# Kernel optimization log

Hardware: AMD Instinct MI355X
Metric: run time of the kernel (lower is better)

## Reference

```python
import jax, jax.numpy as jnp
import numpy as np

NUM_HEADS = 4
NUM_GROUPS = 8
EPS = 1e-5


def setup_inputs() -> dict:
    key = jax.random.key(0)
    ks = jax.random.split(key, 4)
    b, c, h, w = 16, 512, 32, 32
    x = jax.random.normal(ks[0], (b, c, h, w), dtype=jnp.float32)
    norm_gamma = jnp.ones((c,), dtype=jnp.float32)
    norm_beta = jnp.zeros((c,), dtype=jnp.float32)
    qkv_w = jax.random.normal(ks[1], (3 * c, c), dtype=jnp.float32) * (c ** -0.5)
    qkv_b = jnp.zeros((3 * c,), dtype=jnp.float32)
    proj_w = jax.random.normal(ks[2], (c, c), dtype=jnp.float32) * (c ** -0.5)
    proj_b = jnp.zeros((c,), dtype=jnp.float32)
    return {"x": x, "norm_gamma": norm_gamma, "norm_beta": norm_beta,
            "qkv_w": qkv_w, "qkv_b": qkv_b, "proj_w": proj_w, "proj_b": proj_b}


def reference(x, norm_gamma, norm_beta, qkv_w, qkv_b, proj_w, proj_b):
    b, c, h, w = x.shape
    nh = NUM_HEADS
    dh = c // nh
    n = h * w
    # GroupNorm(8, c): normalize over (c/G, h, w) within each group, biased var
    xg = x.reshape(b, NUM_GROUPS, -1)
    mu = jnp.mean(xg, axis=-1, keepdims=True)
    var = jnp.var(xg, axis=-1, keepdims=True)
    xn = ((xg - mu) * jax.lax.rsqrt(var + EPS)).reshape(b, c, h, w)
    xn = xn * norm_gamma[:, None, None] + norm_beta[:, None, None]
    # QKV 1x1 conv == channel matmul
    qkv = jnp.einsum('oc,bchw->bohw', qkv_w, xn) + qkv_b[:, None, None]
    q, k, v = jnp.split(qkv, 3, axis=1)  # each [b, c, h, w]

    def to_heads(t):  # [b, c, h, w] -> [b, nh, n, dh]
        return t.reshape(b, nh, dh, n).transpose(0, 1, 3, 2)

    q, k, v = to_heads(q), to_heads(k), to_heads(v)
    scale = dh ** -0.5
    attn = jax.nn.softmax(jnp.einsum('bhnd,bhmd->bhnm', q, k) * scale, axis=-1)
    out = jnp.einsum('bhnm,bhmd->bhnd', attn, v)  # [b, nh, n, dh]
    out = out.transpose(0, 1, 3, 2).reshape(b, c, h, w)
    out = jnp.einsum('oc,bchw->bohw', proj_w, out) + proj_b[:, None, None]
    return x + out
```

## Files before the change

### kernel.cpp

```cpp
#include <hip/hip_runtime.h>

typedef unsigned short u16;
typedef unsigned int   u32;

typedef __attribute__((ext_vector_type(8)))  short bf16x8;
typedef __attribute__((ext_vector_type(16))) float f32x16;
typedef __attribute__((ext_vector_type(2)))  unsigned int u32x2;
#define MFMA32(a, b, c) __builtin_amdgcn_mfma_f32_32x32x16_bf16(a, b, c, 0, 0, 0)

__device__ __forceinline__ float bf2f(u16 h) { return __uint_as_float(((u32)h) << 16); }
__device__ __forceinline__ u16 f2bf(float f) {
  u32 u = __float_as_uint(f);
  u += 0x7fffu + ((u >> 16) & 1u);
  return (u16)(u >> 16);
}
__device__ __forceinline__ void unpack8(uint4 u, float* f) {
  f[0] = __uint_as_float(u.x << 16); f[1] = __uint_as_float(u.x & 0xffff0000u);
  f[2] = __uint_as_float(u.y << 16); f[3] = __uint_as_float(u.y & 0xffff0000u);
  f[4] = __uint_as_float(u.z << 16); f[5] = __uint_as_float(u.z & 0xffff0000u);
  f[6] = __uint_as_float(u.w << 16); f[7] = __uint_as_float(u.w & 0xffff0000u);
}
__device__ __forceinline__ void unpack4(uint2 u, float* f) {
  f[0] = __uint_as_float(u.x << 16); f[1] = __uint_as_float(u.x & 0xffff0000u);
  f[2] = __uint_as_float(u.y << 16); f[3] = __uint_as_float(u.y & 0xffff0000u);
}

template <bool F>
__device__ __forceinline__ void load8(const void* p, size_t idx, float* f) {
  if constexpr (F) {
    const float4* q = (const float4*)((const float*)p + idx);
    float4 a = q[0], b = q[1];
    f[0] = a.x; f[1] = a.y; f[2] = a.z; f[3] = a.w;
    f[4] = b.x; f[5] = b.y; f[6] = b.z; f[7] = b.w;
  } else {
    unpack8(*(const uint4*)((const u16*)p + idx), f);
  }
}
template <bool F>
__device__ __forceinline__ void load4(const void* p, size_t idx, float* f) {
  if constexpr (F) {
    float4 a = *(const float4*)((const float*)p + idx);
    f[0] = a.x; f[1] = a.y; f[2] = a.z; f[3] = a.w;
  } else {
    unpack4(*(const uint2*)((const u16*)p + idx), f);
  }
}
template <bool F>
__device__ __forceinline__ float load1(const void* p, size_t idx) {
  if constexpr (F) return ((const float*)p)[idx];
  else return bf2f(((const u16*)p)[idx]);
}

__device__ __forceinline__ void gl2lds16(const void* g, void* l) {
  __builtin_amdgcn_global_load_lds(
      (const __attribute__((address_space(1))) void*)g,
      (__attribute__((address_space(3))) void*)l, 16, 0, 0);
}

__global__ void detect_dtype(const void* __restrict__ x, int* __restrict__ flag) {
  if (threadIdx.x == 0 && blockIdx.x == 0) {
    const u32* p = (const u32*)x;
    int sane = 0;
    for (int i = 0; i < 256; ++i) {
      u32 e = (p[i] >> 7) & 0xFFu;
      sane += (e >= 100u && e <= 150u) ? 1 : 0;
    }
    *flag = (sane < 192) ? 1 : 0;
  }
}

__global__ void signal_ws(u16* __restrict__ out, int n) {
  int i = blockIdx.x * 256 + threadIdx.x;
  if (i < n) out[i] = 0x42C8;
}

#define SM_SCALE 0.08838834764831843f
#define QSC 0.12751743f


__global__ void __launch_bounds__(256) wconv_rt(const void* __restrict__ qkvw,
                                                const void* __restrict__ qkvb,
                                                u16* __restrict__ dst,
                                                const int* __restrict__ flag) {
  const bool F = (flag[0] != 0);
  int i = (blockIdx.x * 256 + threadIdx.x) * 8;
  if (i >= 787968) return;
  if (!F) {
    uint4 v = (i < 786432) ? *(const uint4*)((const u16*)qkvw + i)
                           : *(const uint4*)((const u16*)qkvb + (i - 786432));
    *(uint4*)(dst + i) = v;
  } else {
    const float* src = (i < 786432) ? ((const float*)qkvw + i)
                                    : ((const float*)qkvb + (i - 786432));
    float f[8];
    float4 a = *(const float4*)src, b = *(const float4*)(src + 4);
    f[0]=a.x; f[1]=a.y; f[2]=a.z; f[3]=a.w; f[4]=b.x; f[5]=b.y; f[6]=b.z; f[7]=b.w;
    u32 w0 = (u32)f2bf(f[0]) | ((u32)f2bf(f[1]) << 16);
    u32 w1 = (u32)f2bf(f[2]) | ((u32)f2bf(f[3]) << 16);
    u32 w2 = (u32)f2bf(f[4]) | ((u32)f2bf(f[5]) << 16);
    u32 w3 = (u32)f2bf(f[6]) | ((u32)f2bf(f[7]) << 16);
    *(uint4*)(dst + i) = make_uint4(w0, w1, w2, w3);
  }
}

template <bool F>
__device__ __forceinline__ void gn_norm_body(
    const void* __restrict__ x, const void* __restrict__ gamma,
    const void* __restrict__ beta, u16* __restrict__ xT,
    int g, int b, int tid,
    float* ssum, float* ssq, float* scb, float* bsb, float (*Tf)[65]) {
  const size_t base = (size_t)(b * 512 + g * 64) * 1024;
  float sum = 0.f, sq = 0.f;
  for (int i = tid; i < 8192; i += 256) {
    float f[8]; load8<F>(x, base + (size_t)i * 8, f);
#pragma unroll
    for (int m = 0; m < 8; ++m) { sum += f[m]; sq += f[m] * f[m]; }
  }
  ssum[tid] = sum; ssq[tid] = sq; __syncthreads();
  for (int off = 128; off > 0; off >>= 1) {
    if (tid < off) { ssum[tid] += ssum[tid + off]; ssq[tid] += ssq[tid + off]; }
    __syncthreads();
  }
  if (tid < 64) {
    float mu  = ssum[0] * (1.f / 65536.f);
    float var = ssq[0] * (1.f / 65536.f) - mu * mu;
    float s = load1<F>(gamma, g * 64 + tid) * rsqrtf(var + 1e-5f);
    scb[tid] = s;
    bsb[tid] = load1<F>(beta, g * 64 + tid) - mu * s;
  }
  __syncthreads();

  for (int s0 = 0; s0 < 1024; s0 += 64) {
#pragma unroll
    for (int half = 0; half < 2; ++half) {
      int idx = tid + half * 256;
      int c_loc = idx >> 3, s8 = (idx & 7) * 8;
      float f[8];
      load8<F>(x, base + (size_t)c_loc * 1024 + s0 + s8, f);
      float sm = scb[c_loc], ba = bsb[c_loc];
#pragma unroll
      for (int m = 0; m < 8; ++m) Tf[s8 + m][c_loc] = f[m] * sm + ba;
    }
    __syncthreads();
#pragma unroll
    for (int half = 0; half < 2; ++half) {
      int idx = tid + half * 256;
      int s_loc = idx >> 3, c8 = (idx & 7) * 8;
      u32 pk[4];
#pragma unroll
      for (int m = 0; m < 4; ++m)
        pk[m] = (u32)f2bf(Tf[s_loc][c8 + 2 * m]) |
                ((u32)f2bf(Tf[s_loc][c8 + 2 * m + 1]) << 16);
      *(uint4*)(xT + (size_t)(b * 1024 + s0 + s_loc) * 512 + g * 64 + c8) =
          make_uint4(pk[0], pk[1], pk[2], pk[3]);
    }
    __syncthreads();
  }
}

__global__ void __launch_bounds__(256) gn_norm_rt(const void* __restrict__ x,
                                                  const void* __restrict__ gamma,
                                                  const void* __restrict__ beta,
                                                  u16* __restrict__ xT,
                                                  const int* __restrict__ flag) {
  __shared__ float ssum[256], ssq[256], scb[64], bsb[64];
  __shared__ float Tf[64][65];
  const int g = blockIdx.x, b = blockIdx.y, tid = threadIdx.x;
  if (flag[0] != 0) gn_norm_body<true >(x, gamma, beta, xT, g, b, tid, ssum, ssq, scb, bsb, Tf);
  else              gn_norm_body<false>(x, gamma, beta, xT, g, b, tid, ssum, ssq, scb, bsb, Tf);
}

__global__ void __launch_bounds__(256, 4)
gemm_qkv(const u16* __restrict__ xT, const u16* __restrict__ wbf,
         u16* __restrict__ qkT, u16* __restrict__ Vbuf) {
  const bool vrole = (blockIdx.y >= 8);
  const int n0 = blockIdx.x * 128;
  const int m0 = (vrole ? (int)blockIdx.y - 8 : (int)blockIdx.y) * 128;
  const int b  = blockIdx.z;
  __shared__ __align__(16) u16 At[8192];
  __shared__ __align__(16) u16 Bt[8192];
  const int tid = threadIdx.x;
  const int w = tid >> 6, lane = tid & 63;
  const int lo = lane & 31, hi = lane >> 5;
  const int wm = w >> 1, wn = w & 1;
  const u16* bias = wbf + 786432;
  const u16* Ab = vrole ? (wbf + 524288) : (xT + (size_t)b * 524288);
  const u16* Bb = vrole ? (xT + (size_t)b * 524288) : wbf;
  u16* outp = vrole ? (Vbuf + (size_t)b * 524288) : (qkT + (size_t)b * 1048576);
  const int srow = lane >> 3, spc = lane & 7;

  f32x16 cA[2][2];
#pragma unroll
  for (int i = 0; i < 2; ++i)
#pragma unroll
    for (int j = 0; j < 2; ++j)
#pragma unroll
      for (int r = 0; r < 16; ++r) cA[i][j][r] = 0.f;

  for (int kt = 0; kt < 8; ++kt) {
    const int kb = kt * 64;
#pragma unroll
    for (int c = 0; c < 4; ++c) {
      int grp = w * 4 + c;
      int row = grp * 8 + srow;
      int lc  = spc ^ (row & 7);
      gl2lds16(Ab + (size_t)(m0 + row) * 512 + kb + lc * 8, &At[grp * 512]);
      gl2lds16(Bb + (size_t)(n0 + row) * 512 + kb + lc * 8, &Bt[grp * 512]);
    }
    __syncthreads();
#pragma unroll
    for (int k16 = 0; k16 < 4; ++k16) {
      const int lc = k16 * 2 + hi;
      const int rA0 = wm * 64 + lo,  rA1 = rA0 + 32;
      const int rB0 = wn * 64 + lo,  rB1 = rB0 + 32;
      bf16x8 a0 = *(const bf16x8*)&At[rA0 * 64 + ((lc ^ (rA0 & 7)) << 3)];
      bf16x8 a1 = *(const bf16x8*)&At[rA1 * 64 + ((lc ^ (rA1 & 7)) << 3)];
      bf16x8 b0 = *(const bf16x8*)&Bt[rB0 * 64 + ((lc ^ (rB0 & 7)) << 3)];
      bf16x8 b1 = *(const bf16x8*)&Bt[rB1 * 64 + ((lc ^ (rB1 & 7)) << 3)];
      cA[0][0] = MFMA32(a0, b0, cA[0][0]);
      cA[0][1] = MFMA32(a0, b1, cA[0][1]);
      cA[1][0] = MFMA32(a1, b0, cA[1][0]);
      cA[1][1] = MFMA32(a1, b1, cA[1][1]);
    }
    __syncthreads();
  }

  float bcol[2] = {0.f, 0.f};
  if (!vrole) {
    bcol[0] = bf2f(bias[n0 + wn * 64 + lo]);
    bcol[1] = bf2f(bias[n0 + wn * 64 + 32 + lo]);
  }
#pragma unroll
  for (int mt = 0; mt < 2; ++mt)
#pragma unroll
    for (int nt = 0; nt < 2; ++nt) {
      const int nbase = n0 + wn * 64 + nt * 32;
#pragma unroll
      for (int r = 0; r < 16; ++r) {
        int m = m0 + wm * 64 + mt * 32 + (r & 3) + 8 * (r >> 2) + 4 * hi;
        int n = nbase + lo;
        float v = cA[mt][nt][r];
        if (!vrole) {
          v += bcol[nt];
          if (nbase < 512) v *= QSC;
        } else {
          v += bf2f(bias[1024 + m]);
        }
        outp[(size_t)m * 1024 + n] = f2bf(v);
      }
    }
}

template <bool F>
__device__ __forceinline__ void proj_body(const void* __restrict__ A,
                                          const u16* __restrict__ B,
                                          const void* __restrict__ bias,
                                          const void* __restrict__ resid,
                                          void* __restrict__ outp,
                                          int n0, int m0, int b, int tid,
                                          u16 (*At)[72], u16 (*Bt)[72]) {
  const int w = tid >> 6, lane = tid & 63;
  const int lo = lane & 31, hi = lane >> 5;
  const int wm = w >> 1, wn = w & 1;
  const size_t bBase = (size_t)b * 524288;

  f32x16 cA[2][2];
#pragma unroll
  for (int i = 0; i < 2; ++i)
#pragma unroll
    for (int j = 0; j < 2; ++j)
#pragma unroll
      for (int r = 0; r < 16; ++r) cA[i][j][r] = 0.f;

  for (int kt = 0; kt < 8; ++kt) {
#pragma unroll
    for (int i = 0; i < 4; ++i) {
      int idx = tid + i * 256;
      int row = idx >> 3, kc = (idx & 7) * 8;
      int k = kt * 64 + kc;
      {
        if constexpr (F) {
          float f[8]; load8<true>(A, (size_t)(m0 + row) * 512 + k, f);
          u32 w0 = (u32)f2bf(f[0]) | ((u32)f2bf(f[1]) << 16);
          u32 w1 = (u32)f2bf(f[2]) | ((u32)f2bf(f[3]) << 16);
          u32 w2 = (u32)f2bf(f[4]) | ((u32)f2bf(f[5]) << 16);
          u32 w3 = (u32)f2bf(f[6]) | ((u32)f2bf(f[7]) << 16);
          *(uint4*)&At[row][kc] = make_uint4(w0, w1, w2, w3);
        } else {
          *(uint4*)&At[row][kc] =
              *(const uint4*)((const u16*)A + (size_t)(m0 + row) * 512 + k);
        }
      }
      *(uint4*)&Bt[row][kc] =
          *(const uint4*)(B + bBase + (size_t)(n0 + row) * 512 + k);
    }
    __syncthreads();
#pragma unroll
    for (int k16 = 0; k16 < 4; ++k16) {
      const int ko = k16 * 16 + hi * 8;
      bf16x8 a0 = *(const bf16x8*)&At[wm * 64 + lo][ko];
      bf16x8 a1 = *(const bf16x8*)&At[wm * 64 + 32 + lo][ko];
      bf16x8 b0 = *(const bf16x8*)&Bt[wn * 64 + lo][ko];
      bf16x8 b1 = *(const bf16x8*)&Bt[wn * 64 + 32 + lo][ko];
      cA[0][0] = MFMA32(a0, b0, cA[0][0]);
      cA[0][1] = MFMA32(a0, b1, cA[0][1]);
      cA[1][0] = MFMA32(a1, b0, cA[1][0]);
      cA[1][1] = MFMA32(a1, b1, cA[1][1]);
    }
    __syncthreads();
  }

#pragma unroll
  for (int mt = 0; mt < 2; ++mt)
#pragma unroll
    for (int nt = 0; nt < 2; ++nt) {
#pragma unroll
      for (int r = 0; r < 16; ++r) {
        int m = m0 + wm * 64 + mt * 32 + (r & 3) + 8 * (r >> 2) + 4 * hi;
        int n = n0 + wn * 64 + nt * 32 + lo;
        float v = cA[mt][nt][r];
        v += load1<F>(bias, m);
        v += load1<F>(resid, bBase + (size_t)m * 1024 + n);
        size_t off = bBase + (size_t)m * 1024 + n;
        if constexpr (F) ((float*)outp)[off] = v;
        else             ((u16*)outp)[off] = f2bf(v);
      }
    }
}

__global__ void __launch_bounds__(256, 4)
proj_rt(const void* __restrict__ projw, const u16* __restrict__ aout,
        const void* __restrict__ projb, const void* __restrict__ x,
        void* __restrict__ outp, const int* __restrict__ flag) {
  __shared__ __align__(16) u16 At[128][72];
  __shared__ __align__(16) u16 Bt[128][72];
  const int n0 = blockIdx.x * 128, m0 = blockIdx.y * 128, b = blockIdx.z;
  if (flag[0] != 0) proj_body<true >(projw, aout, projb, x, outp, n0, m0, b, threadIdx.x, At, Bt);
  else              proj_body<false>(projw, aout, projb, x, outp, n0, m0, b, threadIdx.x, At, Bt);
}

__global__ void __launch_bounds__(256, 2) attn4(const u16* __restrict__ qkT,
                                                const u16* __restrict__ V,
                                                u16* __restrict__ aout) {
  const int bh = blockIdx.x;
  const int q0 = blockIdx.y * 128;
  const int b = bh >> 2, h = bh & 3;
  const u16* qt = qkT + (size_t)b * 1048576;
  const u16* vb = V + (size_t)b * 524288 + (size_t)(h * 128) * 1024;
  __shared__ __align__(16) u16 smem[32768];
  const int tid = threadIdx.x;
  const int w = tid >> 6, lane = tid & 63;
  const int lo = lane & 31, hi = lane >> 5;

#pragma unroll
  for (int c = 0; c < 8; ++c) {
    int grp = w * 8 + c;
    int row = grp * 4 + (lane >> 4);
    int lc  = (lane & 15) ^ (row & 7);
    gl2lds16(qt + (size_t)(q0 + row) * 1024 + h * 128 + lc * 8, &smem[grp * 512]);
  }
#pragma unroll
  for (int c = 0; c < 4; ++c) {
    int grp = w * 4 + c;
    { int row = grp * 4 + (lane >> 4);
      int lc  = (lane & 15) ^ (row & 7);
      gl2lds16(qt + (size_t)row * 1024 + 512 + h * 128 + lc * 8,
               &smem[16384 + grp * 512]); }
    { int row = grp * 8 + (lane >> 3);
      int lc  = (lane & 7) ^ (row & 7);
      gl2lds16(vb + (size_t)row * 1024 + lc * 8,
               &smem[16384 + 8192 + grp * 512]); }
  }
  __syncthreads();
  bf16x8 qf[8];
  {
    const int row = 32 * w + lo;
#pragma unroll
    for (int k16 = 0; k16 < 8; ++k16) {
      int lc = k16 * 2 + hi;
      qf[k16] = *(const bf16x8*)&smem[row * 128 + ((lc ^ (row & 7)) << 3)];
    }
  }
  __syncthreads();

  f32x16 o[4];
  float lp = 0.f;
#pragma unroll
  for (int dt = 0; dt < 4; ++dt)
#pragma unroll
    for (int r = 0; r < 16; ++r) o[dt][r] = 0.f;

  for (int kt = 0; kt < 16; ++kt) {
    const u16* rb = &smem[((kt & 1) ^ 1) << 14];
    u16* wbuf = &smem[(kt & 1) << 14];

    if (kt < 15) {
      const int k0n = (kt + 1) * 64;
#pragma unroll
      for (int c = 0; c < 4; ++c) {
        int grp = w * 4 + c;
        { int row = grp * 4 + (lane >> 4);
          int lc  = (lane & 15) ^ (row & 7);
          gl2lds16(qt + (size_t)(k0n + row) * 1024 + 512 + h * 128 + lc * 8,
                   wbuf + grp * 512); }
        { int row = grp * 8 + (lane >> 3);
          int lc  = (lane & 7) ^ (row & 7);
          gl2lds16(vb + (size_t)row * 1024 + k0n + lc * 8,
                   wbuf + 8192 + grp * 512); }
      }
    }

    f32x16 s0, s1;
#pragma unroll
    for (int r = 0; r < 16; ++r) { s0[r] = 0.f; s1[r] = 0.f; }
    __builtin_amdgcn_s_setprio(1);
#pragma unroll
    for (int k16 = 0; k16 < 8; ++k16) {
      const int lc = k16 * 2 + hi;
      const int r0 = lo, r1 = lo + 32;
      bf16x8 kf0 = *(const bf16x8*)&rb[r0 * 128 + ((lc ^ (r0 & 7)) << 3)];
      bf16x8 kf1 = *(const bf16x8*)&rb[r1 * 128 + ((lc ^ (r1 & 7)) << 3)];
      s0 = MFMA32(kf0, qf[k16], s0);
      s1 = MFMA32(kf1, qf[k16], s1);
    }
    __builtin_amdgcn_s_setprio(0);

#pragma unroll
    for (int r = 0; r < 16; ++r) {
      s0[r] = exp2f(s0[r]);
      s1[r] = exp2f(s1[r]);
      lp += s0[r] + s1[r];
    }

    bf16x8 pa[4];
#define MKPA(ps, rb0, dst) do {                                               \
      u32 qa0, qa1, qb0, qb1;                                                 \
      asm("v_cvt_pk_bf16_f32 %0, %1, %2" : "=v"(qa0)                          \
          : "v"((ps)[(rb0) + 0]), "v"((ps)[(rb0) + 1]));                      \
      asm("v_cvt_pk_bf16_f32 %0, %1, %2" : "=v"(qa1)                          \
          : "v"((ps)[(rb0) + 2]), "v"((ps)[(rb0) + 3]));                      \
      asm("v_cvt_pk_bf16_f32 %0, %1, %2" : "=v"(qb0)                          \
          : "v"((ps)[(rb0) + 4]), "v"((ps)[(rb0) + 5]));                      \
      asm("v_cvt_pk_bf16_f32 %0, %1, %2" : "=v"(qb1)                          \
          : "v"((ps)[(rb0) + 6]), "v"((ps)[(rb0) + 7]));                      \
      u32x2 r0 = __builtin_amdgcn_permlane32_swap(qa0, qb0, false, false);    \
      u32x2 r1 = __builtin_amdgcn_permlane32_swap(qa1, qb1, false, false);    \
      union { u32 u[4]; bf16x8 v8; } pk_;                                     \
      pk_.u[0] = r0[0]; pk_.u[1] = r1[0]; pk_.u[2] = r0[1]; pk_.u[3] = r1[1]; \
      dst = pk_.v8;                                                           \
    } while (0)
    MKPA(s0, 0, pa[0]);
    MKPA(s0, 8, pa[1]);
    MKPA(s1, 0, pa[2]);
    MKPA(s1, 8, pa[3]);
#undef MKPA

    __builtin_amdgcn_s_setprio(1);
#pragma unroll
    for (int t = 0; t < 4; ++t) {
      const int lc = t * 2 + hi;
#pragma unroll
      for (int dt = 0; dt < 4; ++dt) {
        const int row = dt * 32 + lo;
        bf16x8 bv = *(const bf16x8*)&rb[8192 + row * 64 + ((lc ^ (row & 7)) << 3)];
        o[dt] = MFMA32(pa[t], bv, o[dt]);
      }
    }
    __builtin_amdgcn_s_setprio(0);
    __syncthreads();
  }

  float linv = 1.f / (lp + __shfl_xor(lp, 32));
#pragma unroll
  for (int r = 0; r < 16; ++r) {
    int pat = (r & 3) + 8 * (r >> 2) + 4 * hi;
    float lr = __shfl(linv, pat);
    int q = q0 + 32 * w + pat;
    size_t base = (size_t)(b * 1024 + q) * 512 + h * 128;
    aout[base +  0 + lo] = f2bf(o[0][r] * lr);
    aout[base + 32 + lo] = f2bf(o[1][r] * lr);
    aout[base + 64 + lo] = f2bf(o[2][r] * lr);
    aout[base + 96 + lo] = f2bf(o[3][r] * lr);
  }
}


template <bool F>
__global__ void __launch_bounds__(256) gn_stats(const void* __restrict__ x,
                                                const void* __restrict__ gamma,
                                                const void* __restrict__ beta,
                                                float* __restrict__ sc,
                                                float* __restrict__ bs,
                                                const int* __restrict__ flag) {
  if ((flag[0] != 0) != F) return;
  const int g = blockIdx.x, b = blockIdx.y;
  const int tid = threadIdx.x;
  const size_t base = (size_t)(b * 512 + g * 64) * 1024;
  float sum = 0.f, sq = 0.f;
  for (int i = tid; i < 8192; i += 256) {
    float f[8]; load8<F>(x, base + (size_t)i * 8, f);
#pragma unroll
    for (int m = 0; m < 8; ++m) { sum += f[m]; sq += f[m] * f[m]; }
  }
  __shared__ float ssum[256], ssq[256];
  ssum[tid] = sum; ssq[tid] = sq; __syncthreads();
  for (int off = 128; off > 0; off >>= 1) {
    if (tid < off) { ssum[tid] += ssum[tid + off]; ssq[tid] += ssq[tid + off]; }
    __syncthreads();
  }
  if (tid < 64) {
    float mu  = ssum[0] * (1.f / 65536.f);
    float var = ssq[0] * (1.f / 65536.f) - mu * mu;
    int c = g * 64 + tid;
    float s = load1<F>(gamma, c) * rsqrtf(var + 1e-5f);
    sc[b * 512 + c] = s;
    bs[b * 512 + c] = load1<F>(beta, c) - mu * s;
  }
}

template <bool F, bool BEXT, bool FOUT>
__global__ void __launch_bounds__(256) gemm64(const void* __restrict__ A,
                                              const void* __restrict__ B,
                                              const float* __restrict__ sc,
                                              const float* __restrict__ bs,
                                              const void* __restrict__ bias,
                                              const void* __restrict__ resid,
                                              void* __restrict__ outp,
                                              int mrows, int donorm, int bstride,
                                              const int* __restrict__ flag) {
  if ((flag[0] != 0) != F) return;
  const int s0 = blockIdx.x * 64;
  const int o0 = blockIdx.y * 64;
  const int b  = blockIdx.z;
  __shared__ __align__(16) float At[64][36];
  __shared__ __align__(16) float Bt[64][36];
  const int tid = threadIdx.x;
  const int ty = tid >> 4, tx = tid & 15;
  const int i0 = ty * 4, j0 = tx * 4;
  const int arow = tid >> 2, akc = (tid & 3) * 8;
  const int brow = tid >> 3, bnc = (tid & 7) * 8;
  float acc[4][4] = {};

  for (int kt = 0; kt < 512; kt += 32) {
    float af[8];
    load8<F>(A, (size_t)(o0 + arow) * 512 + akc + kt, af);
    *(float4*)&At[arow][akc]     = make_float4(af[0], af[1], af[2], af[3]);
    *(float4*)&At[arow][akc + 4] = make_float4(af[4], af[5], af[6], af[7]);
    const int c = kt + brow;
    float bf[8];
    load8<(BEXT && F)>(B, (size_t)(b * bstride + c) * 1024 + s0 + bnc, bf);
    float smul = 1.f, badd = 0.f;
    if (donorm) { smul = sc[b * 512 + c]; badd = bs[b * 512 + c]; }
#pragma unroll
    for (int m = 0; m < 8; ++m) Bt[bnc + m][brow] = bf[m] * smul + badd;
    __syncthreads();
#pragma unroll
    for (int kq = 0; kq < 8; ++kq) {
      float4 a0 = *(const float4*)&At[i0 + 0][kq * 4];
      float4 a1 = *(const float4*)&At[i0 + 1][kq * 4];
      float4 a2 = *(const float4*)&At[i0 + 2][kq * 4];
      float4 a3 = *(const float4*)&At[i0 + 3][kq * 4];
      float4 c0 = *(const float4*)&Bt[j0 + 0][kq * 4];
      float4 c1 = *(const float4*)&Bt[j0 + 1][kq * 4];
      float4 c2 = *(const float4*)&Bt[j0 + 2][kq * 4];
      float4 c3 = *(const float4*)&Bt[j0 + 3][kq * 4];
#define DOT4(ii, jj, AV, CV) acc[ii][jj] += AV.x * CV.x + AV.y * CV.y + AV.z * CV.z + AV.w * CV.w;
      DOT4(0,0,a0,c0) DOT4(0,1,a0,c1) DOT4(0,2,a0,c2) DOT4(0,3,a0,c3)
      DOT4(1,0,a1,c0) DOT4(1,1,a1,c1) DOT4(1,2,a1,c2) DOT4(1,3,a1,c3)
      DOT4(2,0,a2,c0) DOT4(2,1,a2,c1) DOT4(2,2,a2,c2) DOT4(2,3,a2,c3)
      DOT4(3,0,a3,c0) DOT4(3,1,a3,c1) DOT4(3,2,a3,c2) DOT4(3,3,a3,c3)
#undef DOT4
    }
    __syncthreads();
  }
#pragma unroll
  for (int ii = 0; ii < 4; ++ii) {
    const int o = o0 + i0 + ii;
    const float bb = load1<F>(bias, o);
    float v[4];
#pragma unroll
    for (int jj = 0; jj < 4; ++jj) v[jj] = acc[ii][jj] + bb;
    if (resid) {
      float xf[4];
      load4<F>(resid, (size_t)(b * 512 + o) * 1024 + s0 + j0, xf);
#pragma unroll
      for (int jj = 0; jj < 4; ++jj) v[jj] += xf[jj];
    }
    const size_t ooff = (size_t)(b * mrows + o) * 1024 + s0 + j0;
    if constexpr (FOUT) {
      *(float4*)((float*)outp + ooff) = make_float4(v[0], v[1], v[2], v[3]);
    } else {
      uint2 pk;
      pk.x = (u32)f2bf(v[0]) | ((u32)f2bf(v[1]) << 16);
      pk.y = (u32)f2bf(v[2]) | ((u32)f2bf(v[3]) << 16);
      *(uint2*)((u16*)outp + ooff) = pk;
    }
  }
}

__global__ void __launch_bounds__(256, 2) attn_old(u16* __restrict__ qkv) {
  const int q0 = blockIdx.x * 128;
  const int bh = blockIdx.y;
  const int b = bh >> 2, h = bh & 3;
  u16* qp = qkv + (size_t)(b * 1536 + h * 128) * 1024;
  const u16* kp = qp + (size_t)512 * 1024;
  const u16* vp = qp + (size_t)1024 * 1024;
  __shared__ __align__(16) u16 Qt[128][136];
  __shared__ __align__(16) u16 Kt[32][136];
  __shared__ __align__(16) u16 Vt[128][40];
  __shared__ __align__(16) u16 Pt[128][40];
  const int tid = threadIdx.x;
  const int w = tid >> 6, lane = tid & 63;
  const int lo = lane & 31, hi = lane >> 5;

  for (int idx = tid; idx < 2048; idx += 256) {
    int d = idx >> 4, s8 = (idx & 15) * 8;
    uint4 qv = *(const uint4*)(qp + (size_t)d * 1024 + q0 + s8);
    const u16* qs = (const u16*)&qv;
#pragma unroll
    for (int m = 0; m < 8; ++m) Qt[s8 + m][d] = qs[m];
  }
  __syncthreads();
  bf16x8 qf[8];
#pragma unroll
  for (int kq = 0; kq < 8; ++kq)
    qf[kq] = *(const bf16x8*)&Qt[32 * w + lo][kq * 16 + hi * 8];

  f32x16 o0, o1, o2, o3;
  float lp[16];
#pragma unroll
  for (int r = 0; r < 16; ++r) { o0[r] = 0.f; o1[r] = 0.f; o2[r] = 0.f; o3[r] = 0.f; lp[r] = 0.f; }

  for (int kt = 0; kt < 32; ++kt) {
    const int k0 = kt * 32;
    __syncthreads();
    for (int idx = tid; idx < 512; idx += 256) {
      int d = idx >> 2, s8 = (idx & 3) * 8;
      uint4 kv = *(const uint4*)(kp + (size_t)d * 1024 + k0 + s8);
      const u16* ks = (const u16*)&kv;
#pragma unroll
      for (int m = 0; m < 8; ++m) Kt[s8 + m][d] = ks[m];
      *(uint4*)&Vt[d][s8] = *(const uint4*)(vp + (size_t)d * 1024 + k0 + s8);
    }
    __syncthreads();
    f32x16 acc;
#pragma unroll
    for (int r = 0; r < 16; ++r) acc[r] = 0.f;
#pragma unroll
    for (int kq = 0; kq < 8; ++kq) {
      bf16x8 bq = *(const bf16x8*)&Kt[lo][kq * 16 + hi * 8];
      acc = MFMA32(qf[kq], bq, acc);
    }
#pragma unroll
    for (int r = 0; r < 16; ++r) {
      float pe = __expf(acc[r] * SM_SCALE);
      lp[r] += pe;
      int row = (r & 3) + 8 * (r >> 2) + 4 * hi;
      Pt[32 * w + row][lo] = f2bf(pe);
    }
    __syncthreads();
#pragma unroll
    for (int kq2 = 0; kq2 < 2; ++kq2) {
      bf16x8 a2 = *(const bf16x8*)&Pt[32 * w + lo][kq2 * 16 + hi * 8];
      bf16x8 b0 = *(const bf16x8*)&Vt[ 0 + lo][kq2 * 16 + hi * 8];
      bf16x8 b1 = *(const bf16x8*)&Vt[32 + lo][kq2 * 16 + hi * 8];
      bf16x8 b2 = *(const bf16x8*)&Vt[64 + lo][kq2 * 16 + hi * 8];
      bf16x8 b3 = *(const bf16x8*)&Vt[96 + lo][kq2 * 16 + hi * 8];
      o0 = MFMA32(a2, b0, o0);
      o1 = MFMA32(a2, b1, o1);
      o2 = MFMA32(a2, b2, o2);
      o3 = MFMA32(a2, b3, o3);
    }
  }
#pragma unroll
  for (int r = 0; r < 16; ++r) {
    float su = lp[r];
    su += __shfl_xor(su, 1);  su += __shfl_xor(su, 2);
    su += __shfl_xor(su, 4);  su += __shfl_xor(su, 8);
    su += __shfl_xor(su, 16);
    float linv = 1.f / su;
    int row = (r & 3) + 8 * (r >> 2) + 4 * hi;
    int q = q0 + 32 * w + row;
    size_t base = (size_t)(b * 1536 + h * 128) * 1024 + q;
    qkv[base + (size_t)( 0 + lo) * 1024] = f2bf(o0[r] * linv);
    qkv[base + (size_t)(32 + lo) * 1024] = f2bf(o1[r] * linv);
    qkv[base + (size_t)(64 + lo) * 1024] = f2bf(o2[r] * linv);
    qkv[base + (size_t)(96 + lo) * 1024] = f2bf(o3[r] * linv);
  }
}

extern "C" void kernel_launch(void* const* d_in, const int* in_sizes, int n_in,
                              void* d_out, int out_size, void* d_ws, size_t ws_size,
                              hipStream_t stream) {
  const void* x     = d_in[0];
  const void* gamma = d_in[1];
  const void* beta  = d_in[2];
  const void* qkvw  = d_in[3];
  const void* qkvb  = d_in[4];
  const void* projw = d_in[5];
  const void* projb = d_in[6];

  char* ws = (char*)d_ws;
  const size_t MB = 1024 * 1024;
  const size_t FAST_NEED = 64 * MB + 64;
  const size_t OLD_NEED  = 48 * MB + 256 + 2 * 16 * 512 * 4;

  if (ws_size >= FAST_NEED) {
    u16* xT   = (u16*)ws;
    u16* qkT  = (u16*)(ws + 16 * MB);
    u16* Vbuf = (u16*)(ws + 48 * MB);
    int* flag = (int*)(ws + 64 * MB);
    u16* wbf  = (u16*)d_out;

    detect_dtype<<<1, 64, 0, stream>>>(x, flag);
    wconv_rt<<<385, 256, 0, stream>>>(qkvw, qkvb, wbf, flag);
    gn_norm_rt<<<dim3(8, 16), 256, 0, stream>>>(x, gamma, beta, xT, flag);

    gemm_qkv<<<dim3(8, 12, 16), 256, 0, stream>>>(xT, wbf, qkT, Vbuf);

    attn4<<<dim3(64, 8), 256, 0, stream>>>(qkT, Vbuf, xT);

    proj_rt<<<dim3(8, 4, 16), 256, 0, stream>>>(projw, xT, projb, x, d_out, flag);
    return;
  }

  if (ws_size < OLD_NEED) {
    signal_ws<<<(out_size + 255) / 256, 256, 0, stream>>>((u16*)d_out, out_size);
    return;
  }

  const size_t QKV_BYTES = (size_t)16 * 1536 * 1024 * 2;
  u16* qkv  = (u16*)ws;
  int* flag = (int*)(ws + QKV_BYTES);
  float* sc = (float*)(ws + QKV_BYTES + 256);
  float* bs = sc + 16 * 512;

  detect_dtype<<<1, 64, 0, stream>>>(x, flag);
  gn_stats<false><<<dim3(8, 16), 256, 0, stream>>>(x, gamma, beta, sc, bs, flag);
  gn_stats<true ><<<dim3(8, 16), 256, 0, stream>>>(x, gamma, beta, sc, bs, flag);
  gemm64<false, true, false><<<dim3(16, 24, 16), 256, 0, stream>>>(
      qkvw, x, sc, bs, qkvb, nullptr, qkv, 1536, 1, 512, flag);
  gemm64<true, true, false><<<dim3(16, 24, 16), 256, 0, stream>>>(
      qkvw, x, sc, bs, qkvb, nullptr, qkv, 1536, 1, 512, flag);
  attn_old<<<dim3(8, 64), 256, 0, stream>>>(qkv);
  gemm64<false, false, false><<<dim3(16, 8, 16), 256, 0, stream>>>(
      projw, qkv, sc, bs, projb, x, d_out, 512, 0, 1536, flag);
  gemm64<true, false, true><<<dim3(16, 8, 16), 256, 0, stream>>>(
      projw, qkv, sc, bs, projb, x, d_out, 512, 0, 1536, flag);
}
```

Baseline: 254.0 us.

## Double-buffer GN transpose tile, remap QKV GEMM blocks across XCDs, drop setprio

The groupnorm transpose stage now double-buffers its shared-memory tile, which lets it drop one barrier per 64-column chunk. The QKV GEMM remaps its linear block index so that consecutive logical tiles land on the same XCD (stride 192 across 8 groups), to improve L2 locality. The s_setprio hints around the MFMA loops in the attention kernel are removed. The tradeoffs are more LDS per GN block and different wave scheduling in attention.

```diff
diff --git a/kernel.cpp b/kernel.cpp
--- a/kernel.cpp
+++ b/kernel.cpp
@@ -108,7 +108,7 @@
     const void* __restrict__ x, const void* __restrict__ gamma,
     const void* __restrict__ beta, u16* __restrict__ xT,
     int g, int b, int tid,
-    float* ssum, float* ssq, float* scb, float* bsb, float (*Tf)[65]) {
+    float* ssum, float* ssq, float* scb, float* bsb, float (*Tf)[64][65]) {
   const size_t base = (size_t)(b * 512 + g * 64) * 1024;
   float sum = 0.f, sq = 0.f;
   for (int i = tid; i < 8192; i += 256) {
@@ -131,6 +131,7 @@
   __syncthreads();
 
   for (int s0 = 0; s0 < 1024; s0 += 64) {
+    const int pb = (s0 >> 6) & 1;
 #pragma unroll
     for (int half = 0; half < 2; ++half) {
       int idx = tid + half * 256;
@@ -139,7 +140,7 @@
       load8<F>(x, base + (size_t)c_loc * 1024 + s0 + s8, f);
       float sm = scb[c_loc], ba = bsb[c_loc];
 #pragma unroll
-      for (int m = 0; m < 8; ++m) Tf[s8 + m][c_loc] = f[m] * sm + ba;
+      for (int m = 0; m < 8; ++m) Tf[pb][s8 + m][c_loc] = f[m] * sm + ba;
     }
     __syncthreads();
 #pragma unroll
@@ -149,12 +150,11 @@
       u32 pk[4];
 #pragma unroll
       for (int m = 0; m < 4; ++m)
-        pk[m] = (u32)f2bf(Tf[s_loc][c8 + 2 * m]) |
-                ((u32)f2bf(Tf[s_loc][c8 + 2 * m + 1]) << 16);
+        pk[m] = (u32)f2bf(Tf[pb][s_loc][c8 + 2 * m]) |
+                ((u32)f2bf(Tf[pb][s_loc][c8 + 2 * m + 1]) << 16);
       *(uint4*)(xT + (size_t)(b * 1024 + s0 + s_loc) * 512 + g * 64 + c8) =
           make_uint4(pk[0], pk[1], pk[2], pk[3]);
     }
-    __syncthreads();
   }
 }
 
@@ -164,7 +164,7 @@
                                                   u16* __restrict__ xT,
                                                   const int* __restrict__ flag) {
   __shared__ float ssum[256], ssq[256], scb[64], bsb[64];
-  __shared__ float Tf[64][65];
+  __shared__ float Tf[2][64][65];
   const int g = blockIdx.x, b = blockIdx.y, tid = threadIdx.x;
   if (flag[0] != 0) gn_norm_body<true >(x, gamma, beta, xT, g, b, tid, ssum, ssq, scb, bsb, Tf);
   else              gn_norm_body<false>(x, gamma, beta, xT, g, b, tid, ssum, ssq, scb, bsb, Tf);
@@ -173,10 +173,16 @@
 __global__ void __launch_bounds__(256, 4)
 gemm_qkv(const u16* __restrict__ xT, const u16* __restrict__ wbf,
          u16* __restrict__ qkT, u16* __restrict__ Vbuf) {
-  const bool vrole = (blockIdx.y >= 8);
-  const int n0 = blockIdx.x * 128;
-  const int m0 = (vrole ? (int)blockIdx.y - 8 : (int)blockIdx.y) * 128;
-  const int b  = blockIdx.z;
+  const int linear  = (int)blockIdx.x + 8 * ((int)blockIdx.y + 12 * (int)blockIdx.z);
+  const int logical = (linear & 7) * 192 + (linear >> 3);
+  const int lx   = logical & 7;
+  const int rest = logical >> 3;
+  const int ly   = rest % 12;
+  const int lz   = rest / 12;
+  const bool vrole = (ly >= 8);
+  const int n0 = lx * 128;
+  const int m0 = (vrole ? ly - 8 : ly) * 128;
+  const int b  = lz;
   __shared__ __align__(16) u16 At[8192];
   __shared__ __align__(16) u16 Bt[8192];
   const int tid = threadIdx.x;
@@ -413,7 +419,6 @@
     f32x16 s0, s1;
 #pragma unroll
     for (int r = 0; r < 16; ++r) { s0[r] = 0.f; s1[r] = 0.f; }
-    __builtin_amdgcn_s_setprio(1);
 #pragma unroll
     for (int k16 = 0; k16 < 8; ++k16) {
       const int lc = k16 * 2 + hi;
@@ -423,7 +428,6 @@
       s0 = MFMA32(kf0, qf[k16], s0);
       s1 = MFMA32(kf1, qf[k16], s1);
     }
-    __builtin_amdgcn_s_setprio(0);
 
 #pragma unroll
     for (int r = 0; r < 16; ++r) {
@@ -455,7 +459,6 @@
     MKPA(s1, 8, pa[3]);
 #undef MKPA
 
-    __builtin_amdgcn_s_setprio(1);
 #pragma unroll
     for (int t = 0; t < 4; ++t) {
       const int lc = t * 2 + hi;
@@ -466,7 +469,6 @@
         o[dt] = MFMA32(pa[t], bv, o[dt]);
       }
     }
-    __builtin_amdgcn_s_setprio(0);
     __syncthreads();
   }
 
```

Result: no change. 249.8 us (-1.7%).
